# Kernel optimization log

Measured on AMD Instinct MI355X. Metric: run time of the kernel, lower is better.

Reference implementation:

```python
import jax, jax.numpy as jnp
import numpy as np

# FNO 2D spectral conv: rfft2 -> keep 2 corner mode blocks -> complex einsum -> scatter -> irfft2
B, H, W, CIN, COUT = 8, 256, 256, 32, 32
M1, M2 = 16, 16
SCALE = 1.0 / (CIN * COUT)  # matches self.scale = 1/(in_channels*out_channels)


def setup_inputs() -> dict:
    key = jax.random.key(0)
    k1, k2, k3 = jax.random.split(key, 3)
    x = jax.random.normal(k1, (B, H, W, CIN), dtype=jnp.float32)  # channels_last input
    wshape = (2, CIN, COUT, M1, M2)  # (2**(ndims-1), in_c, out_c, m1, m2)
    w_real = (jax.random.uniform(k2, wshape, dtype=jnp.float32) * 2.0 - 1.0) * SCALE
    w_imag = (jax.random.uniform(k3, wshape, dtype=jnp.float32) * 2.0 - 1.0) * SCALE
    return {"x": x, "w_real": w_real, "w_imag": w_imag}


def reference(x, w_real, w_imag):
    w = jax.lax.complex(w_real, w_imag)  # complex64 spectral weights
    # channels_last -> channels_first: [B,H,W,C] -> [B,C,H,W]
    xc = jnp.transpose(x, (0, 3, 1, 2))
    x_ft = jnp.fft.rfft2(xc)  # [B, C, H, W//2+1] complex64
    # Two corner blocks along dim H (low and high freqs), low freqs along rfft dim.
    blocks = jnp.stack(
        [x_ft[:, :, :M1, :M2], x_ft[:, :, H - M1:, :M2]], axis=0
    )  # [2, B, Cin, M1, M2]
    # einsum 'wbi...,wio...->w...bo' (reordered here to wbohk; scatter layout equivalent)
    ob = jnp.einsum('wbihk,wiohk->wbohk', blocks, w)  # [2, B, Cout, M1, M2]
    out_ft = jnp.zeros((B, COUT, H, W // 2 + 1), dtype=ob.dtype)
    out_ft = out_ft.at[:, :, :M1, :M2].set(ob[0])
    out_ft = out_ft.at[:, :, H - M1:, :M2].set(ob[1])
    out = jnp.fft.irfft2(out_ft, s=(H, W))  # [B, Cout, H, W] float32
    # back to channels_last; activation is None (identity)
    return jnp.transpose(out, (0, 2, 3, 1))
```

## Files before the change

kernel.cpp:

```cpp
#include <hip/hip_runtime.h>
#include <math.h>


#define INV_HW (1.0f / 65536.0f)

__global__ void k_tw(float* __restrict__ E1, float* __restrict__ U,
                     float* __restrict__ E4) {
  int t = blockIdx.x * blockDim.x + threadIdx.x;
  const float step = 6.28318530717958647692f / 256.0f;
  if (t < 1024) {
    int w = t >> 3, kwp = t & 7;
    int me = (2 * kwp * w) & 255, mo = ((2 * kwp + 1) * w) & 255;
    float se, ce, so, co;
    sincosf(step * (float)me, &se, &ce);
    sincosf(step * (float)mo, &so, &co);
    ((float4*)E1)[t] = make_float4(ce, -se, co, -so);
  } else if (t < 1280) {
    int n = t - 1024;
    float s, c;
    sincosf(step * (float)n, &s, &c);
    ((float2*)U)[n] = make_float2(c, s);
  } else if (t < 2304) {
    int i = t - 1280;
    int w = i >> 3, q = i & 7;
    int me = (2 * q * w) & 255, mo = ((2 * q + 1) * w) & 255;
    float se, ce, so, co;
    sincosf(step * (float)me, &se, &ce);
    sincosf(step * (float)mo, &so, &co);
    float sc_e = (q == 0) ? INV_HW : 2.0f * INV_HW;
    float sc_o = 2.0f * INV_HW;
    ((float4*)E4)[i] = make_float4(sc_e * ce, sc_e * se, sc_o * co, sc_o * so);
  }
}

__global__ __launch_bounds__(256) void k_wdft(const float* __restrict__ x,
                                              const float* __restrict__ E1,
                                              float* __restrict__ T) {
  __shared__ __align__(16) float sx[32 * 260];
  __shared__ float4 sE[1024];
  int bh = blockIdx.x, t = threadIdx.x;
  const float4* e1g = (const float4*)E1;
#pragma unroll
  for (int i = 0; i < 4; ++i) sE[t + 256 * i] = e1g[t + 256 * i];
  const float4* src = (const float4*)(x + (size_t)bh * 8192);
#pragma unroll
  for (int i = 0; i < 8; ++i) {
    int j = t + 256 * i;
    float4 v = src[j];
    int w = j >> 3, c0 = (j & 7) * 4;
    sx[(c0 + 0) * 260 + w] = v.x;
    sx[(c0 + 1) * 260 + w] = v.y;
    sx[(c0 + 2) * 260 + w] = v.z;
    sx[(c0 + 3) * 260 + w] = v.w;
  }
  __syncthreads();
  int c = t >> 3, kwp = t & 7;
  const float* xr = sx + c * 260;
  const float4* eb = sE + kwp;
  float ar = 0, ai = 0, br = 0, bi = 0;
#pragma unroll 4
  for (int j = 0; j < 32; ++j) {
    float4 xa = *(const float4*)(xr + 4 * j);
    float4 xb = *(const float4*)(xr + 128 + 4 * j);
    float4 e0 = eb[(4 * j + 0) * 8];
    float4 e1 = eb[(4 * j + 1) * 8];
    float4 e2 = eb[(4 * j + 2) * 8];
    float4 e3 = eb[(4 * j + 3) * 8];
    float ye, yo;
    ye = xa.x + xb.x; yo = xa.x - xb.x;
    ar += ye * e0.x; ai += ye * e0.y; br += yo * e0.z; bi += yo * e0.w;
    ye = xa.y + xb.y; yo = xa.y - xb.y;
    ar += ye * e1.x; ai += ye * e1.y; br += yo * e1.z; bi += yo * e1.w;
    ye = xa.z + xb.z; yo = xa.z - xb.z;
    ar += ye * e2.x; ai += ye * e2.y; br += yo * e2.z; bi += yo * e2.w;
    ye = xa.w + xb.w; yo = xa.w - xb.w;
    ar += ye * e3.x; ai += ye * e3.y; br += yo * e3.z; bi += yo * e3.w;
  }
  ((float4*)(T + (size_t)bh * 1024))[t] = make_float4(ar, ai, br, bi);
}

__global__ __launch_bounds__(512) void k_hdft(const float* __restrict__ T,
                                              const float* __restrict__ U,
                                              float* __restrict__ X) {
  __shared__ __align__(16) float sT[8192];
  __shared__ float2 sU[256];
  __shared__ float4 sRed[256];
  int b = blockIdx.x >> 5, c = blockIdx.x & 31;
  int t = threadIdx.x;
  const float4* src = (const float4*)(T + (size_t)b * 262144 + c * 32);
  float4* dT = (float4*)sT;
#pragma unroll
  for (int i = 0; i < 4; ++i) {
    int j = t + 512 * i;
    dT[j] = src[(j >> 3) * 256 + (j & 7)];
  }
  if (t < 256) sU[t] = ((const float2*)U)[t];
  __syncthreads();
  int kw = t & 15, kh = (t >> 4) & 15, s = t >> 8;
  float sg = (kh & 1) ? -1.f : 1.f;
  int st1 = kh, st2 = (kh + 240) & 255;
  int ph1 = (st1 * (s * 64)) & 255;
  int ph2 = (st2 * (s * 64)) & 255;
  float x0r = 0, x0i = 0, x1r = 0, x1i = 0;
  int h0 = s * 64;
#pragma unroll 4
  for (int hh = 0; hh < 64; ++hh) {
    int h = h0 + hh;
    float2 t0 = *(const float2*)(sT + h * 32 + kw * 2);
    float2 t1 = *(const float2*)(sT + (h + 128) * 32 + kw * 2);
    float tpx = fmaf(sg, t1.x, t0.x);
    float tpy = fmaf(sg, t1.y, t0.y);
    float2 e1 = sU[ph1];
    float2 e2 = sU[ph2];
    x0r += tpx * e1.x + tpy * e1.y;
    x0i += tpy * e1.x - tpx * e1.y;
    x1r += tpx * e2.x + tpy * e2.y;
    x1i += tpy * e2.x - tpx * e2.y;
    ph1 = (ph1 + st1) & 255;
    ph2 = (ph2 + st2) & 255;
  }
  if (s == 1) sRed[t - 256] = make_float4(x0r, x0i, x1r, x1i);
  __syncthreads();
  if (s == 0) {
    float4 p = sRed[t];
    x0r += p.x; x0i += p.y; x1r += p.z; x1i += p.w;
    float2* Xb = (float2*)(X + (size_t)blockIdx.x * 1024);
    Xb[kh * 16 + kw] = make_float2(x0r, x0i);
    Xb[(kh + 16) * 16 + kw] = make_float2(x1r, x1i);
  }
}

__global__ __launch_bounds__(256) void k_mix(const float* __restrict__ X,
                                             const float* __restrict__ wr,
                                             const float* __restrict__ wi,
                                             float* __restrict__ Y) {
  __shared__ __align__(16) float sX[1024];
  int b = blockIdx.x >> 5, kh = blockIdx.x & 31;
  int blk = kh >> 4, khl = kh & 15;
  int t = threadIdx.x;
  {
    int i = t >> 3, p = t & 7;
    ((float4*)sX)[t] =
        *(const float4*)(X + (size_t)(b * 32 + i) * 1024 + kh * 32 + p * 4);
  }
  __syncthreads();
  int kw = t & 15, o = t >> 4;
  const float* wr0 = wr + (size_t)blk * 262144 + khl * 16 + kw;
  const float* wi0 = wi + (size_t)blk * 262144 + khl * 16 + kw;
  float y0r = 0, y0i = 0, y1r = 0, y1i = 0;
#pragma unroll 4
  for (int i = 0; i < 32; ++i) {
    float2 xv = *(const float2*)(sX + i * 32 + kw * 2);
    float a0 = wr0[i * 8192 + o * 256], b0 = wi0[i * 8192 + o * 256];
    float a1 = wr0[i * 8192 + (o + 16) * 256], b1 = wi0[i * 8192 + (o + 16) * 256];
    y0r += xv.x * a0 - xv.y * b0;
    y0i += xv.x * b0 + xv.y * a0;
    y1r += xv.x * a1 - xv.y * b1;
    y1i += xv.x * b1 + xv.y * a1;
  }
  float2* Yb = (float2*)(Y + (size_t)b * 32768);
  Yb[(o * 32 + kh) * 16 + kw] = make_float2(y0r, y0i);
  Yb[((o + 16) * 32 + kh) * 16 + kw] = make_float2(y1r, y1i);
}

__global__ __launch_bounds__(256) void k_hidft(const float* __restrict__ Y,
                                               const float* __restrict__ U,
                                               float* __restrict__ G) {
  __shared__ __align__(16) float4 sY4[256];
  __shared__ float2 sU[256];
  int bi = blockIdx.x;
  int b = bi >> 7, o = (bi >> 2) & 31, hc = bi & 3;
  int t = threadIdx.x;
  sY4[t] = ((const float4*)(Y + (size_t)(b * 32 + o) * 1024))[t];
  sU[t] = ((const float2*)U)[t];
  __syncthreads();
  int q = t & 7, hl = t >> 3;
  int h = hc * 32 + hl;
  float se0r = 0, se0i = 0, se1r = 0, se1i = 0;
  float so0r = 0, so0i = 0, so1r = 0, so1i = 0;
#pragma unroll 4
  for (int kh2 = 0; kh2 < 16; ++kh2) {
    int khe = 2 * kh2, kho = khe + 1;
    int khae = khe < 16 ? khe : khe + 224;
    int khao = kho < 16 ? kho : kho + 224;
    float2 ee = sU[(khae * h) & 255];
    float2 eo = sU[(khao * h) & 255];
    float4 yE = sY4[khe * 8 + q];
    float4 yO = sY4[kho * 8 + q];
    se0r += yE.x * ee.x - yE.y * ee.y;
    se0i += yE.x * ee.y + yE.y * ee.x;
    se1r += yE.z * ee.x - yE.w * ee.y;
    se1i += yE.z * ee.y + yE.w * ee.x;
    so0r += yO.x * eo.x - yO.y * eo.y;
    so0i += yO.x * eo.y + yO.y * eo.x;
    so1r += yO.z * eo.x - yO.w * eo.y;
    so1i += yO.z * eo.y + yO.w * eo.x;
  }
  float* g0 = G + (((size_t)b * 256 + h) * 32 + o) * 32 + 4 * q;
  float* g1 = G + (((size_t)b * 256 + h + 128) * 32 + o) * 32 + 4 * q;
  *(float4*)g0 = make_float4(se0r + so0r, se0i + so0i, se1r + so1r, se1i + so1i);
  *(float4*)g1 = make_float4(se0r - so0r, se0i - so0i, se1r - so1r, se1i - so1i);
}

__global__ __launch_bounds__(256) void k_widft(const float* __restrict__ G,
                                               const float* __restrict__ E4,
                                               float* __restrict__ out) {
  __shared__ float sG[32 * 33];
  __shared__ float4 sE4[1024];
  int bh = blockIdx.x, t = threadIdx.x;
  const float4* e4g = (const float4*)E4;
#pragma unroll
  for (int i = 0; i < 4; ++i) sE4[t + 256 * i] = e4g[t + 256 * i];
  {
    float4 v = ((const float4*)(G + (size_t)bh * 1024))[t];
    int o = t >> 3, p = t & 7;
    float* d = sG + o * 33 + p * 4;
    d[0] = v.x; d[1] = v.y; d[2] = v.z; d[3] = v.w;
  }
  __syncthreads();
  int o = t & 31, wb = t >> 5;
  float g[32];
#pragma unroll
  for (int k = 0; k < 32; ++k) g[k] = sG[o * 33 + k];
  float* ob = out + (size_t)bh * 8192 + o;
#pragma unroll 2
  for (int j = 0; j < 16; ++j) {
    int w = wb * 16 + j;
    float se = 0.f, so = 0.f;
#pragma unroll
    for (int q = 0; q < 8; ++q) {
      float4 e = sE4[w * 8 + q];
      se += g[4 * q] * e.x - g[4 * q + 1] * e.y;
      so += g[4 * q + 2] * e.z - g[4 * q + 3] * e.w;
    }
    ob[(size_t)w * 32] = se + so;
    ob[(size_t)(w + 128) * 32] = se - so;
  }
}

extern "C" void kernel_launch(void* const* d_in, const int* in_sizes, int n_in,
                              void* d_out, int out_size, void* d_ws, size_t ws_size,
                              hipStream_t stream) {
  const float* x = (const float*)d_in[0];
  const float* wr = (const float*)d_in[1];
  const float* wi = (const float*)d_in[2];
  float* out = (float*)d_out;
  float* ws = (float*)d_ws;

  float* E1 = ws;
  float* U  = ws + 4096;
  float* E4 = ws + 4608;
  float* T  = ws + 8704;
  float* X  = ws + 2105856;
  float* Y  = ws + 2368000;
  float* G  = T;

  k_tw<<<9, 256, 0, stream>>>(E1, U, E4);
  k_wdft<<<2048, 256, 0, stream>>>(x, E1, T);
  k_hdft<<<256, 512, 0, stream>>>(T, U, X);
  k_mix<<<256, 256, 0, stream>>>(X, wr, wi, Y);
  k_hidft<<<1024, 256, 0, stream>>>(Y, U, G);
  k_widft<<<2048, 256, 0, stream>>>(G, E4, out);
}
```

Before: 160.3 us.

## Fuse channel mix with H inverse DFT and restage twiddles through global cache

Combines the spectral channel mix and the inverse H-DFT into one kernel, so Y no longer round-trips through workspace and one launch disappears. The W-DFT now precomputes even/odd butterflies while loading, drops the shared-memory copy of the twiddle table, and writes T in a (b,c,h) layout so the H-DFT reads contiguous rows. The H-DFT uses 1024 threads with a 4-way reduction. The W-inverse kernel reads twiddles straight from global/L1 instead of shared. The trade-off is lower parallelism in the fused kernel (256 blocks) and more cache-dependent twiddle loads.

```diff
diff --git a/kernel.cpp b/kernel.cpp
--- a/kernel.cpp
+++ b/kernel.cpp
@@ -36,75 +36,71 @@
 __global__ __launch_bounds__(256) void k_wdft(const float* __restrict__ x,
                                               const float* __restrict__ E1,
                                               float* __restrict__ T) {
-  __shared__ __align__(16) float sx[32 * 260];
-  __shared__ float4 sE[1024];
+  __shared__ __align__(16) float sxe[32 * 132];
+  __shared__ __align__(16) float sxo[32 * 132];
   int bh = blockIdx.x, t = threadIdx.x;
-  const float4* e1g = (const float4*)E1;
-#pragma unroll
-  for (int i = 0; i < 4; ++i) sE[t + 256 * i] = e1g[t + 256 * i];
   const float4* src = (const float4*)(x + (size_t)bh * 8192);
 #pragma unroll
-  for (int i = 0; i < 8; ++i) {
+  for (int i = 0; i < 4; ++i) {
     int j = t + 256 * i;
-    float4 v = src[j];
+    float4 a = src[j];
+    float4 b = src[j + 1024];
     int w = j >> 3, c0 = (j & 7) * 4;
-    sx[(c0 + 0) * 260 + w] = v.x;
-    sx[(c0 + 1) * 260 + w] = v.y;
-    sx[(c0 + 2) * 260 + w] = v.z;
-    sx[(c0 + 3) * 260 + w] = v.w;
+    sxe[(c0 + 0) * 132 + w] = a.x + b.x;
+    sxe[(c0 + 1) * 132 + w] = a.y + b.y;
+    sxe[(c0 + 2) * 132 + w] = a.z + b.z;
+    sxe[(c0 + 3) * 132 + w] = a.w + b.w;
+    sxo[(c0 + 0) * 132 + w] = a.x - b.x;
+    sxo[(c0 + 1) * 132 + w] = a.y - b.y;
+    sxo[(c0 + 2) * 132 + w] = a.z - b.z;
+    sxo[(c0 + 3) * 132 + w] = a.w - b.w;
   }
   __syncthreads();
   int c = t >> 3, kwp = t & 7;
-  const float* xr = sx + c * 260;
-  const float4* eb = sE + kwp;
+  const float* xe = sxe + c * 132;
+  const float* xo = sxo + c * 132;
+  const float4* eb = ((const float4*)E1) + kwp;
   float ar = 0, ai = 0, br = 0, bi = 0;
 #pragma unroll 4
   for (int j = 0; j < 32; ++j) {
-    float4 xa = *(const float4*)(xr + 4 * j);
-    float4 xb = *(const float4*)(xr + 128 + 4 * j);
+    float4 ye = *(const float4*)(xe + 4 * j);
+    float4 yo = *(const float4*)(xo + 4 * j);
     float4 e0 = eb[(4 * j + 0) * 8];
     float4 e1 = eb[(4 * j + 1) * 8];
     float4 e2 = eb[(4 * j + 2) * 8];
     float4 e3 = eb[(4 * j + 3) * 8];
-    float ye, yo;
-    ye = xa.x + xb.x; yo = xa.x - xb.x;
-    ar += ye * e0.x; ai += ye * e0.y; br += yo * e0.z; bi += yo * e0.w;
-    ye = xa.y + xb.y; yo = xa.y - xb.y;
-    ar += ye * e1.x; ai += ye * e1.y; br += yo * e1.z; bi += yo * e1.w;
-    ye = xa.z + xb.z; yo = xa.z - xb.z;
-    ar += ye * e2.x; ai += ye * e2.y; br += yo * e2.z; bi += yo * e2.w;
-    ye = xa.w + xb.w; yo = xa.w - xb.w;
-    ar += ye * e3.x; ai += ye * e3.y; br += yo * e3.z; bi += yo * e3.w;
-  }
-  ((float4*)(T + (size_t)bh * 1024))[t] = make_float4(ar, ai, br, bi);
-}
-
-__global__ __launch_bounds__(512) void k_hdft(const float* __restrict__ T,
-                                              const float* __restrict__ U,
-                                              float* __restrict__ X) {
+    ar += ye.x * e0.x; ai += ye.x * e0.y; br += yo.x * e0.z; bi += yo.x * e0.w;
+    ar += ye.y * e1.x; ai += ye.y * e1.y; br += yo.y * e1.z; bi += yo.y * e1.w;
+    ar += ye.z * e2.x; ai += ye.z * e2.y; br += yo.z * e2.z; bi += yo.z * e2.w;
+    ar += ye.w * e3.x; ai += ye.w * e3.y; br += yo.w * e3.z; bi += yo.w * e3.w;
+  }
+  int b = bh >> 8, h = bh & 255;
+  ((float4*)(T + ((size_t)(b * 32 + c) * 256 + h) * 32))[kwp] =
+      make_float4(ar, ai, br, bi);
+}
+
+__global__ __launch_bounds__(1024) void k_hdft(const float* __restrict__ T,
+                                               const float* __restrict__ U,
+                                               float* __restrict__ X) {
   __shared__ __align__(16) float sT[8192];
   __shared__ float2 sU[256];
-  __shared__ float4 sRed[256];
-  int b = blockIdx.x >> 5, c = blockIdx.x & 31;
+  __shared__ float4 sRed[768];
   int t = threadIdx.x;
-  const float4* src = (const float4*)(T + (size_t)b * 262144 + c * 32);
+  const float4* src = (const float4*)(T + (size_t)blockIdx.x * 8192);
   float4* dT = (float4*)sT;
-#pragma unroll
-  for (int i = 0; i < 4; ++i) {
-    int j = t + 512 * i;
-    dT[j] = src[(j >> 3) * 256 + (j & 7)];
-  }
+  dT[t] = src[t];
+  dT[t + 1024] = src[t + 1024];
   if (t < 256) sU[t] = ((const float2*)U)[t];
   __syncthreads();
   int kw = t & 15, kh = (t >> 4) & 15, s = t >> 8;
   float sg = (kh & 1) ? -1.f : 1.f;
   int st1 = kh, st2 = (kh + 240) & 255;
-  int ph1 = (st1 * (s * 64)) & 255;
-  int ph2 = (st2 * (s * 64)) & 255;
+  int h0 = s * 32;
+  int ph1 = (st1 * h0) & 255;
+  int ph2 = (st2 * h0) & 255;
   float x0r = 0, x0i = 0, x1r = 0, x1i = 0;
-  int h0 = s * 64;
-#pragma unroll 4
-  for (int hh = 0; hh < 64; ++hh) {
+#pragma unroll 4
+  for (int hh = 0; hh < 32; ++hh) {
     int h = h0 + hh;
     float2 t0 = *(const float2*)(sT + h * 32 + kw * 2);
     float2 t1 = *(const float2*)(sT + (h + 128) * 32 + kw * 2);
@@ -119,98 +115,88 @@
     ph1 = (ph1 + st1) & 255;
     ph2 = (ph2 + st2) & 255;
   }
-  if (s == 1) sRed[t - 256] = make_float4(x0r, x0i, x1r, x1i);
+  if (s > 0) sRed[(s - 1) * 256 + (t & 255)] = make_float4(x0r, x0i, x1r, x1i);
   __syncthreads();
   if (s == 0) {
-    float4 p = sRed[t];
-    x0r += p.x; x0i += p.y; x1r += p.z; x1i += p.w;
+#pragma unroll
+    for (int k = 0; k < 3; ++k) {
+      float4 p = sRed[k * 256 + t];
+      x0r += p.x; x0i += p.y; x1r += p.z; x1i += p.w;
+    }
     float2* Xb = (float2*)(X + (size_t)blockIdx.x * 1024);
     Xb[kh * 16 + kw] = make_float2(x0r, x0i);
     Xb[(kh + 16) * 16 + kw] = make_float2(x1r, x1i);
   }
 }
 
-__global__ __launch_bounds__(256) void k_mix(const float* __restrict__ X,
-                                             const float* __restrict__ wr,
-                                             const float* __restrict__ wi,
-                                             float* __restrict__ Y) {
-  __shared__ __align__(16) float sX[1024];
-  int b = blockIdx.x >> 5, kh = blockIdx.x & 31;
-  int blk = kh >> 4, khl = kh & 15;
+__global__ __launch_bounds__(512) void k_mixidft(const float* __restrict__ X,
+                                                 const float* __restrict__ wr,
+                                                 const float* __restrict__ wi,
+                                                 const float* __restrict__ U,
+                                                 float* __restrict__ G) {
+  __shared__ __align__(16) float2 sY[512];
+  __shared__ float2 sU[256];
+  int b = blockIdx.x >> 5, o = blockIdx.x & 31;
   int t = threadIdx.x;
+  if (t < 256) sU[t] = ((const float2*)U)[t];
   {
-    int i = t >> 3, p = t & 7;
-    ((float4*)sX)[t] =
-        *(const float4*)(X + (size_t)(b * 32 + i) * 1024 + kh * 32 + p * 4);
-  }
-  __syncthreads();
-  int kw = t & 15, o = t >> 4;
-  const float* wr0 = wr + (size_t)blk * 262144 + khl * 16 + kw;
-  const float* wi0 = wi + (size_t)blk * 262144 + khl * 16 + kw;
-  float y0r = 0, y0i = 0, y1r = 0, y1i = 0;
-#pragma unroll 4
-  for (int i = 0; i < 32; ++i) {
-    float2 xv = *(const float2*)(sX + i * 32 + kw * 2);
-    float a0 = wr0[i * 8192 + o * 256], b0 = wi0[i * 8192 + o * 256];
-    float a1 = wr0[i * 8192 + (o + 16) * 256], b1 = wi0[i * 8192 + (o + 16) * 256];
-    y0r += xv.x * a0 - xv.y * b0;
-    y0i += xv.x * b0 + xv.y * a0;
-    y1r += xv.x * a1 - xv.y * b1;
-    y1i += xv.x * b1 + xv.y * a1;
-  }
-  float2* Yb = (float2*)(Y + (size_t)b * 32768);
-  Yb[(o * 32 + kh) * 16 + kw] = make_float2(y0r, y0i);
-  Yb[((o + 16) * 32 + kh) * 16 + kw] = make_float2(y1r, y1i);
-}
-
-__global__ __launch_bounds__(256) void k_hidft(const float* __restrict__ Y,
-                                               const float* __restrict__ U,
-                                               float* __restrict__ G) {
-  __shared__ __align__(16) float4 sY4[256];
-  __shared__ float2 sU[256];
-  int bi = blockIdx.x;
-  int b = bi >> 7, o = (bi >> 2) & 31, hc = bi & 3;
-  int t = threadIdx.x;
-  sY4[t] = ((const float4*)(Y + (size_t)(b * 32 + o) * 1024))[t];
-  sU[t] = ((const float2*)U)[t];
-  __syncthreads();
-  int q = t & 7, hl = t >> 3;
-  int h = hc * 32 + hl;
-  float se0r = 0, se0i = 0, se1r = 0, se1i = 0;
-  float so0r = 0, so0i = 0, so1r = 0, so1i = 0;
-#pragma unroll 4
-  for (int kh2 = 0; kh2 < 16; ++kh2) {
-    int khe = 2 * kh2, kho = khe + 1;
-    int khae = khe < 16 ? khe : khe + 224;
-    int khao = kho < 16 ? kho : kho + 224;
-    float2 ee = sU[(khae * h) & 255];
-    float2 eo = sU[(khao * h) & 255];
-    float4 yE = sY4[khe * 8 + q];
-    float4 yO = sY4[kho * 8 + q];
-    se0r += yE.x * ee.x - yE.y * ee.y;
-    se0i += yE.x * ee.y + yE.y * ee.x;
-    se1r += yE.z * ee.x - yE.w * ee.y;
-    se1i += yE.z * ee.y + yE.w * ee.x;
-    so0r += yO.x * eo.x - yO.y * eo.y;
-    so0i += yO.x * eo.y + yO.y * eo.x;
-    so1r += yO.z * eo.x - yO.w * eo.y;
-    so1i += yO.z * eo.y + yO.w * eo.x;
-  }
-  float* g0 = G + (((size_t)b * 256 + h) * 32 + o) * 32 + 4 * q;
-  float* g1 = G + (((size_t)b * 256 + h + 128) * 32 + o) * 32 + 4 * q;
-  *(float4*)g0 = make_float4(se0r + so0r, se0i + so0i, se1r + so1r, se1i + so1i);
-  *(float4*)g1 = make_float4(se0r - so0r, se0i - so0i, se1r - so1r, se1i - so1i);
+    int kw = t & 15, row = t >> 4;
+    int blk = row >> 4, khl = row & 15;
+    const float* wr0 =
+        wr + (size_t)blk * 262144 + (size_t)o * 256 + khl * 16 + kw;
+    const float* wi0 =
+        wi + (size_t)blk * 262144 + (size_t)o * 256 + khl * 16 + kw;
+    const float* Xb = X + (size_t)b * 32768 + row * 32 + kw * 2;
+    float yr = 0, yi = 0;
+#pragma unroll 4
+    for (int i = 0; i < 32; ++i) {
+      float2 xv = *(const float2*)(Xb + i * 1024);
+      float a = wr0[i * 8192], bb = wi0[i * 8192];
+      yr += xv.x * a - xv.y * bb;
+      yi += xv.x * bb + xv.y * a;
+    }
+    sY[row * 16 + kw] = make_float2(yr, yi);
+  }
+  __syncthreads();
+  const float4* sY4 = (const float4*)sY;
+  int q = t & 7, hr = t >> 3;
+#pragma unroll
+  for (int hb = 0; hb < 2; ++hb) {
+    int h = hr + hb * 64;
+    float se0r = 0, se0i = 0, se1r = 0, se1i = 0;
+    float so0r = 0, so0i = 0, so1r = 0, so1i = 0;
+#pragma unroll 4
+    for (int kh2 = 0; kh2 < 16; ++kh2) {
+      int khe = 2 * kh2, kho = khe + 1;
+      int khae = khe < 16 ? khe : khe + 224;
+      int khao = kho < 16 ? kho : kho + 224;
+      float2 ee = sU[(khae * h) & 255];
+      float2 eo = sU[(khao * h) & 255];
+      float4 yE = sY4[khe * 8 + q];
+      float4 yO = sY4[kho * 8 + q];
+      se0r += yE.x * ee.x - yE.y * ee.y;
+      se0i += yE.x * ee.y + yE.y * ee.x;
+      se1r += yE.z * ee.x - yE.w * ee.y;
+      se1i += yE.z * ee.y + yE.w * ee.x;
+      so0r += yO.x * eo.x - yO.y * eo.y;
+      so0i += yO.x * eo.y + yO.y * eo.x;
+      so1r += yO.z * eo.x - yO.w * eo.y;
+      so1i += yO.z * eo.y + yO.w * eo.x;
+    }
+    float* g0 = G + (((size_t)b * 256 + h) * 32 + o) * 32 + 4 * q;
+    float* g1 = G + (((size_t)b * 256 + h + 128) * 32 + o) * 32 + 4 * q;
+    *(float4*)g0 =
+        make_float4(se0r + so0r, se0i + so0i, se1r + so1r, se1i + so1i);
+    *(float4*)g1 =
+        make_float4(se0r - so0r, se0i - so0i, se1r - so1r, se1i - so1i);
+  }
 }
 
 __global__ __launch_bounds__(256) void k_widft(const float* __restrict__ G,
                                                const float* __restrict__ E4,
                                                float* __restrict__ out) {
   __shared__ float sG[32 * 33];
-  __shared__ float4 sE4[1024];
   int bh = blockIdx.x, t = threadIdx.x;
-  const float4* e4g = (const float4*)E4;
-#pragma unroll
-  for (int i = 0; i < 4; ++i) sE4[t + 256 * i] = e4g[t + 256 * i];
   {
     float4 v = ((const float4*)(G + (size_t)bh * 1024))[t];
     int o = t >> 3, p = t & 7;
@@ -222,6 +208,7 @@
   float g[32];
 #pragma unroll
   for (int k = 0; k < 32; ++k) g[k] = sG[o * 33 + k];
+  const float4* e4g = (const float4*)E4;
   float* ob = out + (size_t)bh * 8192 + o;
 #pragma unroll 2
   for (int j = 0; j < 16; ++j) {
@@ -229,7 +216,7 @@
     float se = 0.f, so = 0.f;
 #pragma unroll
     for (int q = 0; q < 8; ++q) {
-      float4 e = sE4[w * 8 + q];
+      float4 e = e4g[w * 8 + q];
       se += g[4 * q] * e.x - g[4 * q + 1] * e.y;
       so += g[4 * q + 2] * e.z - g[4 * q + 3] * e.w;
     }
@@ -239,8 +226,8 @@
 }
 
 extern "C" void kernel_launch(void* const* d_in, const int* in_sizes, int n_in,
-                              void* d_out, int out_size, void* d_ws, size_t ws_size,
-                              hipStream_t stream) {
+                              void* d_out, int out_size, void* d_ws,
+                              size_t ws_size, hipStream_t stream) {
   const float* x = (const float*)d_in[0];
   const float* wr = (const float*)d_in[1];
   const float* wi = (const float*)d_in[2];
@@ -252,13 +239,11 @@
   float* E4 = ws + 4608;
   float* T  = ws + 8704;
   float* X  = ws + 2105856;
-  float* Y  = ws + 2368000;
   float* G  = T;
 
   k_tw<<<9, 256, 0, stream>>>(E1, U, E4);
   k_wdft<<<2048, 256, 0, stream>>>(x, E1, T);
-  k_hdft<<<256, 512, 0, stream>>>(T, U, X);
-  k_mix<<<256, 256, 0, stream>>>(X, wr, wi, Y);
-  k_hidft<<<1024, 256, 0, stream>>>(Y, U, G);
+  k_hdft<<<256, 1024, 0, stream>>>(T, U, X);
+  k_mixidft<<<256, 512, 0, stream>>>(X, wr, wi, U, G);
   k_widft<<<2048, 256, 0, stream>>>(G, E4, out);
 }
```

After: 192.5 us. 20.1% more time.
